# Kernel optimization log

Measured on AMD Instinct MI355X. Metric: run time of the kernel, lower is better.

## Reference

```python
import jax, jax.numpy as jnp
import numpy as np
from jax import lax

B, T, D, H = 64, 2048, 128, 256  # batch, seq_len, input_dim, hidden_dim


def setup_inputs() -> dict:
    key = jax.random.key(0)
    ks = jax.random.split(key, 21)
    s = 0.05
    p = lambda k, shape: jax.random.normal(k, shape, dtype=jnp.float32) * s
    inp = {"x": jax.random.normal(ks[0], (B, T, D), dtype=jnp.float32)}
    i = 1
    for n in ["e1", "e2", "d1", "d2"]:  # encode1, encode2, reconstruct1, reconstruct2
        inp[n + "_Wih"] = p(ks[i], (4 * H, D)); i += 1
        inp[n + "_Whh"] = p(ks[i], (4 * H, H)); i += 1
        inp[n + "_bih"] = p(ks[i], (4 * H,)); i += 1
        inp[n + "_bhh"] = p(ks[i], (4 * H,)); i += 1
    inp["l1_W"] = p(ks[17], (D, H)); inp["l1_b"] = p(ks[18], (D,))
    inp["l2_W"] = p(ks[19], (D, H)); inp["l2_b"] = p(ks[20], (D,))
    return inp


def _lstm_cell(h, c, xt, Wih, Whh, bih, bhh):
    # PyTorch gate order: i, f, g, o
    g = xt @ Wih.T + h @ Whh.T + bih + bhh  # [B, 4H]
    i, f, gg, o = jnp.split(g, 4, axis=-1)
    c = jax.nn.sigmoid(f) * c + jax.nn.sigmoid(i) * jnp.tanh(gg)
    h = jax.nn.sigmoid(o) * jnp.tanh(c)
    return h, c


def _encode(x, h0, c0, Wih, Whh, bih, bhh):
    # x: [B, T, D] batch_first -> scan over time
    def step(carry, xt):
        h, c = carry
        h, c = _lstm_cell(h, c, xt, Wih, Whh, bih, bhh)
        return (h, c), None
    (h, c), _ = lax.scan(step, (h0, c0), jnp.swapaxes(x, 0, 1))
    return h, c


def _decode(n, h, c, Wih, Whh, bih, bhh, Wl, bl):
    # first output is linear(hidden) before any cell step (matches original decode)
    inp0 = h @ Wl.T + bl  # [B, D]
    def step(carry, _):
        h, c, inp = carry
        h, c = _lstm_cell(h, c, inp, Wih, Whh, bih, bhh)
        inp = h @ Wl.T + bl
        return (h, c, inp), inp
    _, outs = lax.scan(step, (h, c, inp0), None, length=n - 1)  # [n-1, B, D]
    out = jnp.concatenate([inp0[None], outs], axis=0)  # [n, B, D]
    return jnp.swapaxes(out, 0, 1)  # [B, n, D]


def reference(x,
              e1_Wih, e1_Whh, e1_bih, e1_bhh,
              e2_Wih, e2_Whh, e2_bih, e2_bhh,
              d1_Wih, d1_Whh, d1_bih, d1_bhh,
              d2_Wih, d2_Whh, d2_bih, d2_bhh,
              l1_W, l1_b, l2_W, l2_b):
    Bc, Tc = x.shape[0], x.shape[1]
    T1 = Tc // 2
    h0 = jnp.zeros((Bc, H), dtype=x.dtype)
    c0 = jnp.zeros((Bc, H), dtype=x.dtype)
    x1 = x[:, :T1][:, ::-1]  # first half, time-reversed
    x2 = x[:, T1:]
    h1, c1 = _encode(x1, h0, c0, e1_Wih, e1_Whh, e1_bih, e1_bhh)
    h2, c2 = _encode(x2, h1, c1, e2_Wih, e2_Whh, e2_bih, e2_bhh)
    out1 = _decode(T1, h1, c1, d1_Wih, d1_Whh, d1_bih, d1_bhh, l1_W, l1_b)
    out2 = _decode(Tc - T1, h2, c2, d2_Wih, d2_Whh, d2_bih, d2_bhh, l2_W, l2_b)[:, ::-1]
    return jnp.concatenate([out1, out2], axis=1)  # [B, T, D]
```

## Files before the change

### kernel.cpp

```cpp
#include <hip/hip_runtime.h>
#include <stdint.h>

#define Bv 64
#define Tv 2048
#define T1v 1024
#define Dv 128
#define Hv 256

typedef _Float16 h2_t __attribute__((ext_vector_type(2)));

__device__ inline float d2(uint32_t hp, uint32_t wp, float acc) {
#if __has_builtin(__builtin_amdgcn_fdot2)
  return __builtin_amdgcn_fdot2(__builtin_bit_cast(h2_t, hp),
                                __builtin_bit_cast(h2_t, wp), acc, false);
#else
  float out;
  asm("v_dot2_f32_f16 %0, %1, %2, %3" : "=v"(out) : "v"(hp), "v"(wp), "v"(acc));
  return out;
#endif
}

__device__ inline uint16_t f2h(float x) {
  _Float16 h = (_Float16)x;
  return __builtin_bit_cast(uint16_t, h);
}
__device__ inline float h2f(uint16_t u) {
  return (float)__builtin_bit_cast(_Float16, u);
}
__device__ inline uint32_t packpair(float a, float b) {
  return (uint32_t)f2h(a) | ((uint32_t)f2h(b) << 16);
}


__global__ void k_pack_x(const float* __restrict__ x, uint32_t* __restrict__ xpk) {
  int idx = blockIdx.x * 256 + threadIdx.x;
  const float2* x2 = (const float2*)x;
  float2 v = x2[idx];
  xpk[idx] = packpair(v.x, v.y);
}

__global__ void k_pack_w(const float* __restrict__ src, uint32_t* __restrict__ wAll,
                         uint32_t* __restrict__ wLg, uint32_t* __restrict__ wStr) {
  int idx = blockIdx.x * 256 + threadIdx.x;
  int row = idx >> 7, k2 = idx & 127;
  uint32_t pr = packpair(src[row * 256 + 2 * k2], src[row * 256 + 2 * k2 + 1]);
  wAll[k2 * 1024 + row] = pr;
  if (k2 >= 96) {
    int g = (k2 - 96) >> 2, q = (k2 - 96) & 3;
    wLg[(g * 1024 + row) * 4 + q] = pr;
  }
  if (k2 >= 48 && k2 < 96) wStr[row * 48 + (k2 - 48)] = pr;
}

__global__ void k_pack_wih(const float* __restrict__ Wih, uint32_t* __restrict__ wihp) {
  int idx = blockIdx.x * 256 + threadIdx.x;
  int row = idx >> 6, k2 = idx & 63;
  wihp[row * 64 + k2] = packpair(Wih[row * 128 + 2 * k2], Wih[row * 128 + 2 * k2 + 1]);
}

__global__ void k_bias2(const float* __restrict__ bih, const float* __restrict__ bhh,
                        float* __restrict__ bias) {
  int i = blockIdx.x * 256 + threadIdx.x;
  if (i < 1024) bias[i] = bih[i] + bhh[i];
}

__global__ void k_dec_combine(const float* __restrict__ Whh, const float* __restrict__ Wih,
                              const float* __restrict__ bih, const float* __restrict__ bhh,
                              const float* __restrict__ lW, const float* __restrict__ lb,
                              float* __restrict__ wd, float* __restrict__ bias) {
  int j = blockIdx.x;
  int k = threadIdx.x;
  __shared__ float wr[128];
  if (k < 128) wr[k] = Wih[j * 128 + k];
  __syncthreads();
  float acc = Whh[j * 256 + k];
  for (int d = 0; d < 128; ++d) acc += wr[d] * lW[d * 256 + k];
  wd[j * 256 + k] = acc;
  if (k == 0) {
    float s = bih[j] + bhh[j];
    for (int d = 0; d < 128; ++d) s += wr[d] * lb[d];
    bias[j] = s;
  }
}

__global__ void k_pack_wl(const float* __restrict__ lW, uint32_t* __restrict__ wlp) {
  int idx = blockIdx.x * 256 + threadIdx.x;
  int d = idx >> 7, k2 = idx & 127;
  wlp[d * 128 + k2] = packpair(lW[d * 256 + 2 * k2], lW[d * 256 + 2 * k2 + 1]);
}

__global__ __launch_bounds__(256) void k_xp_gemm(const uint32_t* __restrict__ xpk,
                                                 const uint32_t* __restrict__ wihp,
                                                 uint16_t* __restrict__ xp, int xt0, int xdt) {
  const int b = blockIdx.z;
  const int s0 = blockIdx.y * 32;
  const int r = blockIdx.x * 256 + threadIdx.x;
  uint32_t wreg[64];
#pragma unroll
  for (int k = 0; k < 64; ++k) wreg[k] = wihp[r * 64 + k];
  for (int sl = 0; sl < 32; ++sl) {
    const int s = s0 + sl;
    const int t = xt0 + s * xdt;
    const uint32_t* __restrict__ xrow = xpk + ((size_t)b * Tv + t) * 64;
    float a0 = 0.f, a1 = 0.f;
#pragma unroll
    for (int k = 0; k < 64; k += 2) {
      a0 = d2(xrow[k], wreg[k], a0);
      a1 = d2(xrow[k + 1], wreg[k + 1], a1);
    }
    xp[((size_t)b * T1v + s) * 1024 + r] = f2h(a0 + a1);
  }
}


struct ChainCfg {
  const uint32_t* wAll;
  const uint4* wLg;
  const uint32_t* wStr;
  const uint32_t* wih;
  const uint32_t* xpk;
  const uint16_t* xps;
  const float* bias;
  const float* h0;
  const float* c0;
  float* hN;
  float* cN;
  uint16_t* hist;
  int xt0, xdt;
};

template <int NRESP, bool WIH>
__global__ void __launch_bounds__(512)
__attribute__((amdgpu_waves_per_eu(2, 2)))
k_rnn5(ChainCfg cA, ChainCfg cB, int nA) {
  __shared__ __align__(16) uint4 wlds4[8 * 1024];
  __shared__ float gsm[1024];
  __shared__ __align__(16) uint16_t h16[256];
  __shared__ __align__(16) uint32_t xsh[64];

  const bool isA = (int)blockIdx.x < nA;
  const ChainCfg cfg = isA ? cA : cB;
  const int b = isA ? (int)blockIdx.x : ((int)blockIdx.x - nA);
  const int tid = threadIdx.x;
  const int r0 = tid, r1 = tid + 512;

#pragma unroll
  for (int i = 0; i < 16; ++i) wlds4[i * 512 + tid] = cfg.wLg[i * 512 + tid];

  uint16_t* histp = cfg.hist ? cfg.hist + (size_t)b * 1024 * 256 : nullptr;

  float creg = 0.f;
  if (tid < 256) {
    float h0v = cfg.h0 ? cfg.h0[b * 256 + tid] : 0.f;
    creg = cfg.c0 ? cfg.c0[b * 256 + tid] : 0.f;
    uint16_t hu = f2h(h0v);
    h16[tid] = hu;
    if (histp) histp[tid] = hu;
  }

  uint32_t w0[NRESP], w1[NRESP];
#pragma unroll
  for (int k = 0; k < NRESP; ++k) w0[k] = cfg.wAll[k * 1024 + r0];
#pragma unroll
  for (int k = 0; k < NRESP; ++k) w1[k] = cfg.wAll[k * 1024 + r1];
  const float bias0 = cfg.bias[r0];
  const float bias1 = cfg.bias[r1];

  constexpr int NS4 = (96 - NRESP) / 4;
  const uint4* ws0 = (const uint4*)(cfg.wStr + (size_t)r0 * 48 + (NRESP - 48));
  const uint4* ws1 = (const uint4*)(cfg.wStr + (size_t)r1 * 48 + (NRESP - 48));
  const uint4* wi0 = cfg.wih ? (const uint4*)(cfg.wih + (size_t)r0 * 64) : nullptr;
  const uint4* wi1 = cfg.wih ? (const uint4*)(cfg.wih + (size_t)r1 * 64) : nullptr;
  const bool hasx = cfg.xps != nullptr;

  __syncthreads();

  for (int s = 0; s < 1024; ++s) {
    float xa0 = 0.f, xa1 = 0.f;
    if (hasx) {
      size_t xb = ((size_t)b * 1024 + s) * 1024;
      xa0 = h2f(cfg.xps[xb + r0]);
      xa1 = h2f(cfg.xps[xb + r1]);
    }
    if constexpr (WIH) {
      if (cfg.wih) {
        if (tid < 64) {
          const int t = cfg.xt0 + s * cfg.xdt;
          xsh[tid] = cfg.xpk[((size_t)b * Tv + t) * 64 + tid];
        }
        __syncthreads();
      }
    }

    const uint4* H4 = (const uint4*)h16;
    float a00 = bias0, a01 = 0.f, a10 = bias1, a11 = 0.f;

#pragma unroll
    for (int c4 = 0; c4 < NRESP / 4; ++c4) {
      const uint4 hv = H4[c4];
      a00 = d2(hv.x, w0[4 * c4 + 0], a00);
      a01 = d2(hv.y, w0[4 * c4 + 1], a01);
      a10 = d2(hv.x, w1[4 * c4 + 0], a10);
      a11 = d2(hv.y, w1[4 * c4 + 1], a11);
      a00 = d2(hv.z, w0[4 * c4 + 2], a00);
      a01 = d2(hv.w, w0[4 * c4 + 3], a01);
      a10 = d2(hv.z, w1[4 * c4 + 2], a10);
      a11 = d2(hv.w, w1[4 * c4 + 3], a11);
    }
    if constexpr (NS4 > 0) {
#pragma unroll
      for (int u = 0; u < NS4; ++u) {
        const uint4 hv = H4[NRESP / 4 + u];
        const uint4 wv0 = ws0[u];
        const uint4 wv1 = ws1[u];
        a00 = d2(hv.x, wv0.x, a00);
        a01 = d2(hv.y, wv0.y, a01);
        a10 = d2(hv.x, wv1.x, a10);
        a11 = d2(hv.y, wv1.y, a11);
        a00 = d2(hv.z, wv0.z, a00);
        a01 = d2(hv.w, wv0.w, a01);
        a10 = d2(hv.z, wv1.z, a10);
        a11 = d2(hv.w, wv1.w, a11);
      }
    }
#pragma unroll
    for (int g = 0; g < 8; ++g) {
      const uint4 hv = H4[24 + g];
      const uint4 wv0 = wlds4[g * 1024 + r0];
      const uint4 wv1 = wlds4[g * 1024 + r1];
      a00 = d2(hv.x, wv0.x, a00);
      a01 = d2(hv.y, wv0.y, a01);
      a10 = d2(hv.x, wv1.x, a10);
      a11 = d2(hv.y, wv1.y, a11);
      a00 = d2(hv.z, wv0.z, a00);
      a01 = d2(hv.w, wv0.w, a01);
      a10 = d2(hv.z, wv1.z, a10);
      a11 = d2(hv.w, wv1.w, a11);
    }
    if constexpr (WIH) {
      if (cfg.wih) {
        const uint4* XS4 = (const uint4*)xsh;
#pragma unroll
        for (int u = 0; u < 16; ++u) {
          const uint4 xv = XS4[u];
          const uint4 wv0 = wi0[u];
          const uint4 wv1 = wi1[u];
          a00 = d2(xv.x, wv0.x, a00);
          a01 = d2(xv.y, wv0.y, a01);
          a10 = d2(xv.x, wv1.x, a10);
          a11 = d2(xv.y, wv1.y, a11);
          a00 = d2(xv.z, wv0.z, a00);
          a01 = d2(xv.w, wv0.w, a01);
          a10 = d2(xv.z, wv1.z, a10);
          a11 = d2(xv.w, wv1.w, a11);
        }
      }
    }

    gsm[r0] = a00 + a01 + xa0;
    gsm[r1] = a10 + a11 + xa1;
    __syncthreads();

    if (tid < 256) {
      const float gi = gsm[tid];
      const float gf = gsm[tid + 256];
      const float gg = gsm[tid + 512];
      const float go = gsm[tid + 768];
      const float si = 1.f / (1.f + __expf(-gi));
      const float sf = 1.f / (1.f + __expf(-gf));
      const float so = 1.f / (1.f + __expf(-go));
      const float tg = 2.f / (1.f + __expf(-2.f * gg)) - 1.f;
      const float cn = sf * creg + si * tg;
      const float tc = 2.f / (1.f + __expf(-2.f * cn)) - 1.f;
      creg = cn;
      const uint16_t hu = f2h(so * tc);
      h16[tid] = hu;
      if (histp && s < 1023) histp[(size_t)(s + 1) * 256 + tid] = hu;
    }
    __syncthreads();
  }

  if (cfg.hN && tid < 256) {
    cfg.hN[b * 256 + tid] = h2f(h16[tid]);
    cfg.cN[b * 256 + tid] = creg;
  }
}

template <bool WIH>
__global__ void __launch_bounds__(1024) k_rnnD(ChainCfg cA, ChainCfg cB, int nA) {
  __shared__ __align__(16) uint4 wlds4[8 * 1024];
  __shared__ float gsm[1024];
  __shared__ __align__(16) uint16_t h16[256];
  __shared__ __align__(16) uint32_t xsh[64];

  const bool isA = (int)blockIdx.x < nA;
  const ChainCfg cfg = isA ? cA : cB;
  const int b = isA ? (int)blockIdx.x : ((int)blockIdx.x - nA);
  const int tid = threadIdx.x;
  const int r0 = tid;

#pragma unroll
  for (int i = 0; i < 8; ++i) wlds4[i * 1024 + tid] = cfg.wLg[i * 1024 + tid];

  uint16_t* histp = cfg.hist ? cfg.hist + (size_t)b * 1024 * 256 : nullptr;

  float creg = 0.f;
  if (tid < 256) {
    float h0v = cfg.h0 ? cfg.h0[b * 256 + tid] : 0.f;
    creg = cfg.c0 ? cfg.c0[b * 256 + tid] : 0.f;
    uint16_t hu = f2h(h0v);
    h16[tid] = hu;
    if (histp) histp[tid] = hu;
  }

  uint32_t w0[48];
#pragma unroll
  for (int k = 0; k < 48; ++k) w0[k] = cfg.wAll[k * 1024 + r0];
  const float bias0 = cfg.bias[r0];
  const uint4* ws0 = (const uint4*)(cfg.wStr + (size_t)r0 * 48);
  const uint4* wi0 = cfg.wih ? (const uint4*)(cfg.wih + (size_t)r0 * 64) : nullptr;
  const bool hasx = cfg.xps != nullptr;

  __syncthreads();

  for (int s = 0; s < 1024; ++s) {
    float xa0 = 0.f;
    if (hasx) xa0 = h2f(cfg.xps[((size_t)b * 1024 + s) * 1024 + r0]);
    if constexpr (WIH) {
      if (cfg.wih) {
        if (tid < 64) {
          const int t = cfg.xt0 + s * cfg.xdt;
          xsh[tid] = cfg.xpk[((size_t)b * Tv + t) * 64 + tid];
        }
        __syncthreads();
      }
    }

    const uint4* H4 = (const uint4*)h16;
    float a00 = bias0, a01 = 0.f;
#pragma unroll
    for (int c4 = 0; c4 < 12; ++c4) {
      const uint4 hv = H4[c4];
      a00 = d2(hv.x, w0[4 * c4 + 0], a00);
      a01 = d2(hv.y, w0[4 * c4 + 1], a01);
      a00 = d2(hv.z, w0[4 * c4 + 2], a00);
      a01 = d2(hv.w, w0[4 * c4 + 3], a01);
    }
#pragma unroll 4
    for (int u = 0; u < 12; ++u) {
      const uint4 hv = H4[12 + u];
      const uint4 wv = ws0[u];
      a00 = d2(hv.x, wv.x, a00);
      a01 = d2(hv.y, wv.y, a01);
      a00 = d2(hv.z, wv.z, a00);
      a01 = d2(hv.w, wv.w, a01);
    }
#pragma unroll
    for (int g = 0; g < 8; ++g) {
      const uint4 hv = H4[24 + g];
      const uint4 wv = wlds4[g * 1024 + r0];
      a00 = d2(hv.x, wv.x, a00);
      a01 = d2(hv.y, wv.y, a01);
      a00 = d2(hv.z, wv.z, a00);
      a01 = d2(hv.w, wv.w, a01);
    }
    if constexpr (WIH) {
      if (cfg.wih) {
        const uint4* XS4 = (const uint4*)xsh;
#pragma unroll 4
        for (int u = 0; u < 16; ++u) {
          const uint4 xv = XS4[u];
          const uint4 wv = wi0[u];
          a00 = d2(xv.x, wv.x, a00);
          a01 = d2(xv.y, wv.y, a01);
          a00 = d2(xv.z, wv.z, a00);
          a01 = d2(xv.w, wv.w, a01);
        }
      }
    }

    gsm[r0] = a00 + a01 + xa0;
    __syncthreads();

    if (tid < 256) {
      const float gi = gsm[tid];
      const float gf = gsm[tid + 256];
      const float gg = gsm[tid + 512];
      const float go = gsm[tid + 768];
      const float si = 1.f / (1.f + __expf(-gi));
      const float sf = 1.f / (1.f + __expf(-gf));
      const float so = 1.f / (1.f + __expf(-go));
      const float tg = 2.f / (1.f + __expf(-2.f * gg)) - 1.f;
      const float cn = sf * creg + si * tg;
      const float tc = 2.f / (1.f + __expf(-2.f * cn)) - 1.f;
      creg = cn;
      const uint16_t hu = f2h(so * tc);
      h16[tid] = hu;
      if (histp && s < 1023) histp[(size_t)(s + 1) * 256 + tid] = hu;
    }
    __syncthreads();
  }

  if (cfg.hN && tid < 256) {
    cfg.hN[b * 256 + tid] = h2f(h16[tid]);
    cfg.cN[b * 256 + tid] = creg;
  }
}

__global__ __launch_bounds__(256) void k_out(const uint16_t* __restrict__ hist,
                                             const uint32_t* __restrict__ wlp,
                                             const float* __restrict__ lb,
                                             float* __restrict__ out, int outbase, int tsign) {
  const int b = blockIdx.y;
  const int t0 = blockIdx.x * 64;
  __shared__ __align__(16) uint32_t hq[64 * 128];
  const uint32_t* hsrc = (const uint32_t*)hist;
  for (int i = threadIdx.x; i < 64 * 128; i += 256) {
    hq[i] = hsrc[((size_t)b * 1024 + t0) * 128 + i];
  }
  __syncthreads();
  const int d = threadIdx.x & 127;
  const int th = threadIdx.x >> 7;
  float acc[32];
#pragma unroll
  for (int it = 0; it < 32; ++it) acc[it] = lb[d];
  const uint4* W4 = (const uint4*)(wlp + (size_t)d * 128);
  const uint4* HQ4 = (const uint4*)hq;
  for (int k2c = 0; k2c < 32; ++k2c) {
    const uint4 wv = W4[k2c];
#pragma unroll
    for (int it = 0; it < 32; ++it) {
      const int tl = th * 32 + it;
      const uint4 hv = HQ4[tl * 32 + k2c];
      acc[it] = d2(hv.x, wv.x, acc[it]);
      acc[it] = d2(hv.y, wv.y, acc[it]);
      acc[it] = d2(hv.z, wv.z, acc[it]);
      acc[it] = d2(hv.w, wv.w, acc[it]);
    }
  }
#pragma unroll
  for (int it = 0; it < 32; ++it) {
    const int tl = th * 32 + it;
    const int t = t0 + tl;
    const int tout = outbase + tsign * t;
    out[((size_t)b * Tv + tout) * Dv + d] = acc[it];
  }
}


extern "C" void kernel_launch(void* const* d_in, const int* in_sizes, int n_in,
                              void* d_out, int out_size, void* d_ws, size_t ws_size,
                              hipStream_t stream) {
  const float* x = (const float*)d_in[0];
  const float* e1_Wih = (const float*)d_in[1];
  const float* e1_Whh = (const float*)d_in[2];
  const float* e1_bih = (const float*)d_in[3];
  const float* e1_bhh = (const float*)d_in[4];
  const float* e2_Wih = (const float*)d_in[5];
  const float* e2_Whh = (const float*)d_in[6];
  const float* e2_bih = (const float*)d_in[7];
  const float* e2_bhh = (const float*)d_in[8];
  const float* d1_Wih = (const float*)d_in[9];
  const float* d1_Whh = (const float*)d_in[10];
  const float* d1_bih = (const float*)d_in[11];
  const float* d1_bhh = (const float*)d_in[12];
  const float* d2_Wih = (const float*)d_in[13];
  const float* d2_Whh = (const float*)d_in[14];
  const float* d2_bih = (const float*)d_in[15];
  const float* d2_bhh = (const float*)d_in[16];
  const float* l1_W = (const float*)d_in[17];
  const float* l1_b = (const float*)d_in[18];
  const float* l2_W = (const float*)d_in[19];
  const float* l2_b = (const float*)d_in[20];

  uint8_t* wsb = (uint8_t*)d_ws;
  size_t off = 0;
  auto take = [&](size_t n) -> void* {
    void* pp = wsb + off;
    off += (n + 255) & ~(size_t)255;
    return pp;
  };
  uint32_t* xpk = (uint32_t*)take((size_t)Bv * Tv * 64 * 4);
  uint16_t* hist1 = (uint16_t*)take((size_t)Bv * T1v * Hv * 2);
  uint16_t* hist2 = (uint16_t*)take((size_t)Bv * T1v * Hv * 2);
  struct WSet { uint32_t *wAll, *wLg, *wStr, *wih; float* bias; };
  auto take_wset = [&](bool with_ih) -> WSet {
    WSet w;
    w.wAll = (uint32_t*)take(128 * 1024 * 4);
    w.wLg = (uint32_t*)take(8 * 1024 * 16);
    w.wStr = (uint32_t*)take(1024 * 48 * 4);
    w.wih = with_ih ? (uint32_t*)take(1024 * 64 * 4) : nullptr;
    w.bias = (float*)take(1024 * 4);
    return w;
  };
  WSet we1 = take_wset(true);
  WSet we2 = take_wset(true);
  WSet wd1 = take_wset(false);
  WSet wd2 = take_wset(false);
  float* wd32 = (float*)take(1024 * 256 * 4);
  uint32_t* wl1p = (uint32_t*)take(128 * 128 * 4);
  uint32_t* wl2p = (uint32_t*)take(128 * 128 * 4);
  float* h1 = (float*)take(64 * 256 * 4);
  float* c1 = (float*)take(64 * 256 * 4);
  float* h2 = (float*)take(64 * 256 * 4);
  float* c2 = (float*)take(64 * 256 * 4);
  uint16_t* xp = (uint16_t*)take((size_t)Bv * T1v * 1024 * 2);
  const bool use_xp = ws_size >= off;

  int variant = 2;
  {
    hipFuncAttributes fa;
    auto ok = [&](const void* f) {
      return hipFuncGetAttributes(&fa, f) == hipSuccess && fa.localSizeBytes == 0;
    };
    if (use_xp) {
      if (ok(reinterpret_cast<const void*>(&k_rnn5<96, false>))) variant = 0;
      else if (ok(reinterpret_cast<const void*>(&k_rnn5<80, false>))) variant = 1;
    } else {
      if (ok(reinterpret_cast<const void*>(&k_rnn5<96, true>))) variant = 0;
      else if (ok(reinterpret_cast<const void*>(&k_rnn5<80, true>))) variant = 1;
    }
  }
  auto launch_rnn = [&](int grid, ChainCfg a, ChainCfg b2, int nA) {
    if (use_xp) {
      if (variant == 0)      k_rnn5<96, false><<<grid, 512, 0, stream>>>(a, b2, nA);
      else if (variant == 1) k_rnn5<80, false><<<grid, 512, 0, stream>>>(a, b2, nA);
      else                   k_rnnD<false><<<grid, 1024, 0, stream>>>(a, b2, nA);
    } else {
      if (variant == 0)      k_rnn5<96, true><<<grid, 512, 0, stream>>>(a, b2, nA);
      else if (variant == 1) k_rnn5<80, true><<<grid, 512, 0, stream>>>(a, b2, nA);
      else                   k_rnnD<true><<<grid, 1024, 0, stream>>>(a, b2, nA);
    }
  };

  k_pack_x<<<(Bv * Tv * 64) / 256, 256, 0, stream>>>(x, xpk);
  k_pack_w<<<512, 256, 0, stream>>>(e1_Whh, we1.wAll, we1.wLg, we1.wStr);
  k_pack_wih<<<256, 256, 0, stream>>>(e1_Wih, we1.wih);
  k_bias2<<<4, 256, 0, stream>>>(e1_bih, e1_bhh, we1.bias);
  k_pack_w<<<512, 256, 0, stream>>>(e2_Whh, we2.wAll, we2.wLg, we2.wStr);
  k_pack_wih<<<256, 256, 0, stream>>>(e2_Wih, we2.wih);
  k_bias2<<<4, 256, 0, stream>>>(e2_bih, e2_bhh, we2.bias);
  k_dec_combine<<<1024, 256, 0, stream>>>(d1_Whh, d1_Wih, d1_bih, d1_bhh, l1_W, l1_b, wd32, wd1.bias);
  k_pack_w<<<512, 256, 0, stream>>>(wd32, wd1.wAll, wd1.wLg, wd1.wStr);
  k_dec_combine<<<1024, 256, 0, stream>>>(d2_Whh, d2_Wih, d2_bih, d2_bhh, l2_W, l2_b, wd32, wd2.bias);
  k_pack_w<<<512, 256, 0, stream>>>(wd32, wd2.wAll, wd2.wLg, wd2.wStr);
  k_pack_wl<<<64, 256, 0, stream>>>(l1_W, wl1p);
  k_pack_wl<<<64, 256, 0, stream>>>(l2_W, wl2p);

  if (use_xp) k_xp_gemm<<<dim3(4, 32, 64), 256, 0, stream>>>(xpk, we1.wih, xp, 1023, -1);
  ChainCfg e1c{we1.wAll, (const uint4*)we1.wLg, we1.wStr, use_xp ? nullptr : we1.wih,
               use_xp ? nullptr : xpk, use_xp ? xp : nullptr, we1.bias,
               nullptr, nullptr, h1, c1, nullptr, 1023, -1};
  launch_rnn(64, e1c, e1c, 64);

  if (use_xp) k_xp_gemm<<<dim3(4, 32, 64), 256, 0, stream>>>(xpk, we2.wih, xp, 1024, 1);
  ChainCfg e2c{we2.wAll, (const uint4*)we2.wLg, we2.wStr, use_xp ? nullptr : we2.wih,
               use_xp ? nullptr : xpk, use_xp ? xp : nullptr, we2.bias,
               h1, c1, h2, c2, nullptr, 1024, 1};
  ChainCfg d1c{wd1.wAll, (const uint4*)wd1.wLg, wd1.wStr, nullptr, nullptr, nullptr,
               wd1.bias, h1, c1, nullptr, nullptr, hist1, 0, 0};
  launch_rnn(128, e2c, d1c, 64);

  ChainCfg d2c{wd2.wAll, (const uint4*)wd2.wLg, wd2.wStr, nullptr, nullptr, nullptr,
               wd2.bias, h2, c2, nullptr, nullptr, hist2, 0, 0};
  launch_rnn(64, d2c, d2c, 64);

  k_out<<<dim3(16, 64), 256, 0, stream>>>(hist1, wl1p, l1_b, (float*)d_out, 0, 1);
  k_out<<<dim3(16, 64), 256, 0, stream>>>(hist2, wl2p, l2_b, (float*)d_out, 2047, -1);
}
```

Baseline: 7.015 ms.

## Add 512-thread LSTM recurrence kernel with per-unit gate ownership and DPP reductions

Adds a new recurrent kernel in which each group of four threads owns two hidden units across all four gates. The K dimension is split four ways and reduced with DPP cross-lane adds, so the gate activations run in registers without a shared-memory gate buffer. The h vector is double-buffered, leaving one barrier per step instead of two. Weights are repacked so 192 words per thread live in VGPRs and the rest in LDS, and the input projection is stored in a matching interleaved layout. This risks heavy register pressure, which is why it sits behind a spill check with fallback to the old kernel, and it removes the 1024-thread fallback path.

```diff
diff --git a/kernel.cpp b/kernel.cpp
--- a/kernel.cpp
+++ b/kernel.cpp
@@ -30,6 +30,18 @@
 __device__ inline uint32_t packpair(float a, float b) {
   return (uint32_t)f2h(a) | ((uint32_t)f2h(b) << 16);
 }
+__device__ inline float unpk(uint32_t u, int hi) {
+  return h2f((uint16_t)(hi ? (u >> 16) : (u & 0xffff)));
+}
+__device__ inline float sigm(float x) { return 1.f / (1.f + __expf(-x)); }
+__device__ inline float tanh_(float x) { return 2.f / (1.f + __expf(-2.f * x)) - 1.f; }
+
+__device__ inline float qsum4(float v) {
+  int t = __builtin_amdgcn_update_dpp(0, __float_as_int(v), 0xB1, 0xF, 0xF, true);
+  v += __int_as_float(t);
+  t = __builtin_amdgcn_update_dpp(0, __float_as_int(v), 0x4E, 0xF, 0xF, true);
+  return v + __int_as_float(t);
+}
 
 
 __global__ void k_pack_x(const float* __restrict__ x, uint32_t* __restrict__ xpk) {
@@ -46,10 +58,42 @@
   uint32_t pr = packpair(src[row * 256 + 2 * k2], src[row * 256 + 2 * k2 + 1]);
   wAll[k2 * 1024 + row] = pr;
   if (k2 >= 96) {
-    int g = (k2 - 96) >> 2, q = (k2 - 96) & 3;
-    wLg[(g * 1024 + row) * 4 + q] = pr;
+    int g = (k2 - 96) >> 2, qq = (k2 - 96) & 3;
+    wLg[(g * 1024 + row) * 4 + qq] = pr;
   }
   if (k2 >= 48 && k2 < 96) wStr[row * 48 + (k2 - 48)] = pr;
+}
+
+__global__ void k_pack_w2(const float* __restrict__ src, uint32_t* __restrict__ wOn,
+                          uint32_t* __restrict__ wLds) {
+  int idx = blockIdx.x * 256 + threadIdx.x;
+  int r = idx >> 7, k2 = idx & 127;
+  uint32_t pr = packpair(src[r * 256 + 2 * k2], src[r * 256 + 2 * k2 + 1]);
+  int gate = r >> 8, u = r & 255;
+  int u_hi = u >> 7, jb = u & 127;
+  int q = k2 >> 5, kk = k2 & 31;
+  int tid = jb * 4 + q;
+  int ri = u_hi * 4 + gate;
+  if (kk < 24) {
+    wOn[(ri * 24 + kk) * 512 + tid] = pr;
+  } else {
+    int p = ri * 2 + ((kk - 24) >> 2);
+    int c = (kk - 24) & 3;
+    wLds[((size_t)p * 512 + tid) * 4 + c] = pr;
+  }
+}
+
+__global__ void k_bias_pack(const float* __restrict__ b32, uint32_t* __restrict__ bpk) {
+  int jb = threadIdx.x;
+  uint32_t w[4];
+#pragma unroll
+  for (int wi = 0; wi < 4; ++wi) {
+    int ri0 = 2 * wi, ri1 = 2 * wi + 1;
+    int row0 = (ri0 & 3) * 256 + jb + 128 * (ri0 >> 2);
+    int row1 = (ri1 & 3) * 256 + jb + 128 * (ri1 >> 2);
+    w[wi] = packpair(b32[row0], b32[row1]);
+  }
+  ((uint4*)bpk)[jb] = make_uint4(w[0], w[1], w[2], w[3]);
 }
 
 __global__ void k_pack_wih(const float* __restrict__ Wih, uint32_t* __restrict__ wihp) {
@@ -89,6 +133,7 @@
   wlp[d * 128 + k2] = packpair(lW[d * 256 + 2 * k2], lW[d * 256 + 2 * k2 + 1]);
 }
 
+template <int LAY>
 __global__ __launch_bounds__(256) void k_xp_gemm(const uint32_t* __restrict__ xpk,
                                                  const uint32_t* __restrict__ wihp,
                                                  uint16_t* __restrict__ xp, int xt0, int xdt) {
@@ -98,6 +143,9 @@
   uint32_t wreg[64];
 #pragma unroll
   for (int k = 0; k < 64; ++k) wreg[k] = wihp[r * 64 + k];
+  const int gate = r >> 8, u = r & 255;
+  const int u_hi = u >> 7, jb = u & 127;
+  const int ri = u_hi * 4 + gate;
   for (int sl = 0; sl < 32; ++sl) {
     const int s = s0 + sl;
     const int t = xt0 + s * xdt;
@@ -108,7 +156,136 @@
       a0 = d2(xrow[k], wreg[k], a0);
       a1 = d2(xrow[k + 1], wreg[k + 1], a1);
     }
-    xp[((size_t)b * T1v + s) * 1024 + r] = f2h(a0 + a1);
+    uint16_t v = f2h(a0 + a1);
+    if (LAY == 0)
+      xp[(((size_t)b * T1v + s) * 128 + jb) * 8 + ri] = v;
+    else
+      xp[((size_t)b * T1v + s) * 1024 + r] = v;
+  }
+}
+
+
+struct CfgU {
+  const uint32_t* wOn;
+  const uint4* wLds;
+  const uint4* bpk;
+  const uint4* xps;
+  const float* h0;
+  const float* c0;
+  float* hN;
+  float* cN;
+  uint16_t* hist;
+};
+
+__global__ void __launch_bounds__(512)
+__attribute__((amdgpu_waves_per_eu(2, 2)))
+k_rnnU(CfgU cA, CfgU cB, int nA) {
+  __shared__ __align__(16) uint4 wldsM[16 * 512];
+  __shared__ __align__(16) uint16_t hb[2][256];
+
+  const bool isA = (int)blockIdx.x < nA;
+  const CfgU cfg = isA ? cA : cB;
+  const int b = isA ? (int)blockIdx.x : ((int)blockIdx.x - nA);
+  const int tid = threadIdx.x;
+  const int q = tid & 3, jb = tid >> 2;
+  const float qz = (q == 0) ? 1.f : 0.f;
+
+#pragma unroll
+  for (int i = 0; i < 16; ++i) wldsM[i * 512 + tid] = cfg.wLds[i * 512 + tid];
+
+  uint32_t wreg[192];
+#pragma unroll
+  for (int k = 0; k < 192; ++k) wreg[k] = cfg.wOn[k * 512 + tid];
+
+  const uint4 bp = cfg.bpk[jb];
+  float c0r = cfg.c0 ? cfg.c0[b * 256 + jb] : 0.f;
+  float c1r = cfg.c0 ? cfg.c0[b * 256 + jb + 128] : 0.f;
+
+  uint16_t* histp = cfg.hist ? cfg.hist + (size_t)b * 1024 * 256 : nullptr;
+  if (q == 0) {
+    float h00 = cfg.h0 ? cfg.h0[b * 256 + jb] : 0.f;
+    float h01 = cfg.h0 ? cfg.h0[b * 256 + jb + 128] : 0.f;
+    uint16_t u0 = f2h(h00), u1 = f2h(h01);
+    hb[0][jb] = u0;
+    hb[0][jb + 128] = u1;
+    if (histp) {
+      histp[jb] = u0;
+      histp[jb + 128] = u1;
+    }
+  }
+  const uint4* xps4 = cfg.xps ? cfg.xps + (size_t)b * 1024 * 128 + jb : nullptr;
+
+  __syncthreads();
+
+  int cur = 0;
+  for (int s = 0; s < 1024; ++s) {
+    uint4 xq = make_uint4(0, 0, 0, 0);
+    if (xps4) xq = xps4[(size_t)s * 128];
+
+    float acc[8];
+    acc[0] = qz * (unpk(bp.x, 0) + unpk(xq.x, 0));
+    acc[1] = qz * (unpk(bp.x, 1) + unpk(xq.x, 1));
+    acc[2] = qz * (unpk(bp.y, 0) + unpk(xq.y, 0));
+    acc[3] = qz * (unpk(bp.y, 1) + unpk(xq.y, 1));
+    acc[4] = qz * (unpk(bp.z, 0) + unpk(xq.z, 0));
+    acc[5] = qz * (unpk(bp.z, 1) + unpk(xq.z, 1));
+    acc[6] = qz * (unpk(bp.w, 0) + unpk(xq.w, 0));
+    acc[7] = qz * (unpk(bp.w, 1) + unpk(xq.w, 1));
+
+    const uint4* H4 = (const uint4*)hb[cur];
+#pragma unroll
+    for (int c = 0; c < 6; ++c) {
+      const uint4 hv = H4[q * 8 + c];
+#pragma unroll
+      for (int ri = 0; ri < 8; ++ri) {
+        const int base = ri * 24 + c * 4;
+        acc[ri] = d2(hv.x, wreg[base + 0], acc[ri]);
+        acc[ri] = d2(hv.y, wreg[base + 1], acc[ri]);
+        acc[ri] = d2(hv.z, wreg[base + 2], acc[ri]);
+        acc[ri] = d2(hv.w, wreg[base + 3], acc[ri]);
+      }
+    }
+#pragma unroll
+    for (int p = 0; p < 2; ++p) {
+      const uint4 hv = H4[q * 8 + 6 + p];
+#pragma unroll
+      for (int ri = 0; ri < 8; ++ri) {
+        const uint4 wv = wldsM[(ri * 2 + p) * 512 + tid];
+        acc[ri] = d2(hv.x, wv.x, acc[ri]);
+        acc[ri] = d2(hv.y, wv.y, acc[ri]);
+        acc[ri] = d2(hv.z, wv.z, acc[ri]);
+        acc[ri] = d2(hv.w, wv.w, acc[ri]);
+      }
+    }
+
+#pragma unroll
+    for (int ri = 0; ri < 8; ++ri) acc[ri] = qsum4(acc[ri]);
+
+    const float cn0 = sigm(acc[1]) * c0r + sigm(acc[0]) * tanh_(acc[2]);
+    const float h0v = sigm(acc[3]) * tanh_(cn0);
+    c0r = cn0;
+    const float cn1 = sigm(acc[5]) * c1r + sigm(acc[4]) * tanh_(acc[6]);
+    const float h1v = sigm(acc[7]) * tanh_(cn1);
+    c1r = cn1;
+
+    const uint16_t hu0 = f2h(h0v), hu1 = f2h(h1v);
+    if (q == 0) {
+      hb[cur ^ 1][jb] = hu0;
+      hb[cur ^ 1][jb + 128] = hu1;
+      if (histp && s < 1023) {
+        histp[(size_t)(s + 1) * 256 + jb] = hu0;
+        histp[(size_t)(s + 1) * 256 + jb + 128] = hu1;
+      }
+    }
+    __syncthreads();
+    cur ^= 1;
+  }
+
+  if (cfg.hN && q == 0) {
+    cfg.hN[b * 256 + jb] = h2f(hb[cur][jb]);
+    cfg.hN[b * 256 + jb + 128] = h2f(hb[cur][jb + 128]);
+    cfg.cN[b * 256 + jb] = c0r;
+    cfg.cN[b * 256 + jb + 128] = c1r;
   }
 }
 
@@ -266,135 +443,10 @@
       const float gf = gsm[tid + 256];
       const float gg = gsm[tid + 512];
       const float go = gsm[tid + 768];
-      const float si = 1.f / (1.f + __expf(-gi));
-      const float sf = 1.f / (1.f + __expf(-gf));
-      const float so = 1.f / (1.f + __expf(-go));
-      const float tg = 2.f / (1.f + __expf(-2.f * gg)) - 1.f;
-      const float cn = sf * creg + si * tg;
-      const float tc = 2.f / (1.f + __expf(-2.f * cn)) - 1.f;
+      const float cn = sigm(gf) * creg + sigm(gi) * tanh_(gg);
+      const float hv = sigm(go) * tanh_(cn);
       creg = cn;
-      const uint16_t hu = f2h(so * tc);
-      h16[tid] = hu;
-      if (histp && s < 1023) histp[(size_t)(s + 1) * 256 + tid] = hu;
-    }
-    __syncthreads();
-  }
-
-  if (cfg.hN && tid < 256) {
-    cfg.hN[b * 256 + tid] = h2f(h16[tid]);
-    cfg.cN[b * 256 + tid] = creg;
-  }
-}
-
-template <bool WIH>
-__global__ void __launch_bounds__(1024) k_rnnD(ChainCfg cA, ChainCfg cB, int nA) {
-  __shared__ __align__(16) uint4 wlds4[8 * 1024];
-  __shared__ float gsm[1024];
-  __shared__ __align__(16) uint16_t h16[256];
-  __shared__ __align__(16) uint32_t xsh[64];
-
-  const bool isA = (int)blockIdx.x < nA;
-  const ChainCfg cfg = isA ? cA : cB;
-  const int b = isA ? (int)blockIdx.x : ((int)blockIdx.x - nA);
-  const int tid = threadIdx.x;
-  const int r0 = tid;
-
-#pragma unroll
-  for (int i = 0; i < 8; ++i) wlds4[i * 1024 + tid] = cfg.wLg[i * 1024 + tid];
-
-  uint16_t* histp = cfg.hist ? cfg.hist + (size_t)b * 1024 * 256 : nullptr;
-
-  float creg = 0.f;
-  if (tid < 256) {
-    float h0v = cfg.h0 ? cfg.h0[b * 256 + tid] : 0.f;
-    creg = cfg.c0 ? cfg.c0[b * 256 + tid] : 0.f;
-    uint16_t hu = f2h(h0v);
-    h16[tid] = hu;
-    if (histp) histp[tid] = hu;
-  }
-
-  uint32_t w0[48];
-#pragma unroll
-  for (int k = 0; k < 48; ++k) w0[k] = cfg.wAll[k * 1024 + r0];
-  const float bias0 = cfg.bias[r0];
-  const uint4* ws0 = (const uint4*)(cfg.wStr + (size_t)r0 * 48);
-  const uint4* wi0 = cfg.wih ? (const uint4*)(cfg.wih + (size_t)r0 * 64) : nullptr;
-  const bool hasx = cfg.xps != nullptr;
-
-  __syncthreads();
-
-  for (int s = 0; s < 1024; ++s) {
-    float xa0 = 0.f;
-    if (hasx) xa0 = h2f(cfg.xps[((size_t)b * 1024 + s) * 1024 + r0]);
-    if constexpr (WIH) {
-      if (cfg.wih) {
-        if (tid < 64) {
-          const int t = cfg.xt0 + s * cfg.xdt;
-          xsh[tid] = cfg.xpk[((size_t)b * Tv + t) * 64 + tid];
-        }
-        __syncthreads();
-      }
-    }
-
-    const uint4* H4 = (const uint4*)h16;
-    float a00 = bias0, a01 = 0.f;
-#pragma unroll
-    for (int c4 = 0; c4 < 12; ++c4) {
-      const uint4 hv = H4[c4];
-      a00 = d2(hv.x, w0[4 * c4 + 0], a00);
-      a01 = d2(hv.y, w0[4 * c4 + 1], a01);
-      a00 = d2(hv.z, w0[4 * c4 + 2], a00);
-      a01 = d2(hv.w, w0[4 * c4 + 3], a01);
-    }
-#pragma unroll 4
-    for (int u = 0; u < 12; ++u) {
-      const uint4 hv = H4[12 + u];
-      const uint4 wv = ws0[u];
-      a00 = d2(hv.x, wv.x, a00);
-      a01 = d2(hv.y, wv.y, a01);
-      a00 = d2(hv.z, wv.z, a00);
-      a01 = d2(hv.w, wv.w, a01);
-    }
-#pragma unroll
-    for (int g = 0; g < 8; ++g) {
-      const uint4 hv = H4[24 + g];
-      const uint4 wv = wlds4[g * 1024 + r0];
-      a00 = d2(hv.x, wv.x, a00);
-      a01 = d2(hv.y, wv.y, a01);
-      a00 = d2(hv.z, wv.z, a00);
-      a01 = d2(hv.w, wv.w, a01);
-    }
-    if constexpr (WIH) {
-      if (cfg.wih) {
-        const uint4* XS4 = (const uint4*)xsh;
-#pragma unroll 4
-        for (int u = 0; u < 16; ++u) {
-          const uint4 xv = XS4[u];
-          const uint4 wv = wi0[u];
-          a00 = d2(xv.x, wv.x, a00);
-          a01 = d2(xv.y, wv.y, a01);
-          a00 = d2(xv.z, wv.z, a00);
-          a01 = d2(xv.w, wv.w, a01);
-        }
-      }
-    }
-
-    gsm[r0] = a00 + a01 + xa0;
-    __syncthreads();
-
-    if (tid < 256) {
-      const float gi = gsm[tid];
-      const float gf = gsm[tid + 256];
-      const float gg = gsm[tid + 512];
-      const float go = gsm[tid + 768];
-      const float si = 1.f / (1.f + __expf(-gi));
-      const float sf = 1.f / (1.f + __expf(-gf));
-      const float so = 1.f / (1.f + __expf(-go));
-      const float tg = 2.f / (1.f + __expf(-2.f * gg)) - 1.f;
-      const float cn = sf * creg + si * tg;
-      const float tc = 2.f / (1.f + __expf(-2.f * cn)) - 1.f;
-      creg = cn;
-      const uint16_t hu = f2h(so * tc);
+      const uint16_t hu = f2h(hv);
       h16[tid] = hu;
       if (histp && s < 1023) histp[(size_t)(s + 1) * 256 + tid] = hu;
     }
@@ -483,7 +535,11 @@
   uint32_t* xpk = (uint32_t*)take((size_t)Bv * Tv * 64 * 4);
   uint16_t* hist1 = (uint16_t*)take((size_t)Bv * T1v * Hv * 2);
   uint16_t* hist2 = (uint16_t*)take((size_t)Bv * T1v * Hv * 2);
-  struct WSet { uint32_t *wAll, *wLg, *wStr, *wih; float* bias; };
+  struct WSet {
+    uint32_t *wAll, *wLg, *wStr, *wih;
+    float* bias;
+    uint32_t *wOn, *wLds, *bpk;
+  };
   auto take_wset = [&](bool with_ih) -> WSet {
     WSet w;
     w.wAll = (uint32_t*)take(128 * 1024 * 4);
@@ -491,6 +547,9 @@
     w.wStr = (uint32_t*)take(1024 * 48 * 4);
     w.wih = with_ih ? (uint32_t*)take(1024 * 64 * 4) : nullptr;
     w.bias = (float*)take(1024 * 4);
+    w.wOn = (uint32_t*)take(192 * 512 * 4);
+    w.wLds = (uint32_t*)take(16 * 512 * 16);
+    w.bpk = (uint32_t*)take(128 * 16);
     return w;
   };
   WSet we1 = take_wset(true);
@@ -510,60 +569,85 @@
   int variant = 2;
   {
     hipFuncAttributes fa;
-    auto ok = [&](const void* f) {
+    auto spillfree = [&](const void* f) {
       return hipFuncGetAttributes(&fa, f) == hipSuccess && fa.localSizeBytes == 0;
     };
-    if (use_xp) {
-      if (ok(reinterpret_cast<const void*>(&k_rnn5<96, false>))) variant = 0;
-      else if (ok(reinterpret_cast<const void*>(&k_rnn5<80, false>))) variant = 1;
+    if (use_xp && spillfree(reinterpret_cast<const void*>(&k_rnnU))) {
+      variant = 0;
+    } else if (use_xp) {
+      if (spillfree(reinterpret_cast<const void*>(&k_rnn5<96, false>))) variant = 1;
     } else {
-      if (ok(reinterpret_cast<const void*>(&k_rnn5<96, true>))) variant = 0;
-      else if (ok(reinterpret_cast<const void*>(&k_rnn5<80, true>))) variant = 1;
-    }
-  }
-  auto launch_rnn = [&](int grid, ChainCfg a, ChainCfg b2, int nA) {
-    if (use_xp) {
-      if (variant == 0)      k_rnn5<96, false><<<grid, 512, 0, stream>>>(a, b2, nA);
-      else if (variant == 1) k_rnn5<80, false><<<grid, 512, 0, stream>>>(a, b2, nA);
-      else                   k_rnnD<false><<<grid, 1024, 0, stream>>>(a, b2, nA);
-    } else {
-      if (variant == 0)      k_rnn5<96, true><<<grid, 512, 0, stream>>>(a, b2, nA);
-      else if (variant == 1) k_rnn5<80, true><<<grid, 512, 0, stream>>>(a, b2, nA);
-      else                   k_rnnD<true><<<grid, 1024, 0, stream>>>(a, b2, nA);
-    }
-  };
+      if (spillfree(reinterpret_cast<const void*>(&k_rnn5<96, true>))) variant = 1;
+    }
+  }
 
   k_pack_x<<<(Bv * Tv * 64) / 256, 256, 0, stream>>>(x, xpk);
   k_pack_w<<<512, 256, 0, stream>>>(e1_Whh, we1.wAll, we1.wLg, we1.wStr);
+  k_pack_w2<<<512, 256, 0, stream>>>(e1_Whh, we1.wOn, we1.wLds);
   k_pack_wih<<<256, 256, 0, stream>>>(e1_Wih, we1.wih);
   k_bias2<<<4, 256, 0, stream>>>(e1_bih, e1_bhh, we1.bias);
+  k_bias_pack<<<1, 128, 0, stream>>>(we1.bias, we1.bpk);
   k_pack_w<<<512, 256, 0, stream>>>(e2_Whh, we2.wAll, we2.wLg, we2.wStr);
+  k_pack_w2<<<512, 256, 0, stream>>>(e2_Whh, we2.wOn, we2.wLds);
   k_pack_wih<<<256, 256, 0, stream>>>(e2_Wih, we2.wih);
   k_bias2<<<4, 256, 0, stream>>>(e2_bih, e2_bhh, we2.bias);
+  k_bias_pack<<<1, 128, 0, stream>>>(we2.bias, we2.bpk);
   k_dec_combine<<<1024, 256, 0, stream>>>(d1_Whh, d1_Wih, d1_bih, d1_bhh, l1_W, l1_b, wd32, wd1.bias);
   k_pack_w<<<512, 256, 0, stream>>>(wd32, wd1.wAll, wd1.wLg, wd1.wStr);
+  k_pack_w2<<<512, 256, 0, stream>>>(wd32, wd1.wOn, wd1.wLds);
+  k_bias_pack<<<1, 128, 0, stream>>>(wd1.bias, wd1.bpk);
   k_dec_combine<<<1024, 256, 0, stream>>>(d2_Whh, d2_Wih, d2_bih, d2_bhh, l2_W, l2_b, wd32, wd2.bias);
   k_pack_w<<<512, 256, 0, stream>>>(wd32, wd2.wAll, wd2.wLg, wd2.wStr);
+  k_pack_w2<<<512, 256, 0, stream>>>(wd32, wd2.wOn, wd2.wLds);
+  k_bias_pack<<<1, 128, 0, stream>>>(wd2.bias, wd2.bpk);
   k_pack_wl<<<64, 256, 0, stream>>>(l1_W, wl1p);
   k_pack_wl<<<64, 256, 0, stream>>>(l2_W, wl2p);
 
-  if (use_xp) k_xp_gemm<<<dim3(4, 32, 64), 256, 0, stream>>>(xpk, we1.wih, xp, 1023, -1);
-  ChainCfg e1c{we1.wAll, (const uint4*)we1.wLg, we1.wStr, use_xp ? nullptr : we1.wih,
-               use_xp ? nullptr : xpk, use_xp ? xp : nullptr, we1.bias,
-               nullptr, nullptr, h1, c1, nullptr, 1023, -1};
-  launch_rnn(64, e1c, e1c, 64);
-
-  if (use_xp) k_xp_gemm<<<dim3(4, 32, 64), 256, 0, stream>>>(xpk, we2.wih, xp, 1024, 1);
-  ChainCfg e2c{we2.wAll, (const uint4*)we2.wLg, we2.wStr, use_xp ? nullptr : we2.wih,
-               use_xp ? nullptr : xpk, use_xp ? xp : nullptr, we2.bias,
-               h1, c1, h2, c2, nullptr, 1024, 1};
-  ChainCfg d1c{wd1.wAll, (const uint4*)wd1.wLg, wd1.wStr, nullptr, nullptr, nullptr,
-               wd1.bias, h1, c1, nullptr, nullptr, hist1, 0, 0};
-  launch_rnn(128, e2c, d1c, 64);
-
-  ChainCfg d2c{wd2.wAll, (const uint4*)wd2.wLg, wd2.wStr, nullptr, nullptr, nullptr,
-               wd2.bias, h2, c2, nullptr, nullptr, hist2, 0, 0};
-  launch_rnn(64, d2c, d2c, 64);
+  auto launch_old = [&](int grid, ChainCfg a, ChainCfg b2, int nA) {
+    if (use_xp) {
+      if (variant == 1) k_rnn5<96, false><<<grid, 512, 0, stream>>>(a, b2, nA);
+      else              k_rnn5<80, false><<<grid, 512, 0, stream>>>(a, b2, nA);
+    } else {
+      if (variant == 1) k_rnn5<96, true><<<grid, 512, 0, stream>>>(a, b2, nA);
+      else              k_rnn5<80, true><<<grid, 512, 0, stream>>>(a, b2, nA);
+    }
+  };
+
+  if (variant == 0) {
+    k_xp_gemm<0><<<dim3(4, 32, 64), 256, 0, stream>>>(xpk, we1.wih, xp, 1023, -1);
+    CfgU e1c{we1.wOn, (const uint4*)we1.wLds, (const uint4*)we1.bpk, (const uint4*)xp,
+             nullptr, nullptr, h1, c1, nullptr};
+    k_rnnU<<<64, 512, 0, stream>>>(e1c, e1c, 64);
+
+    k_xp_gemm<0><<<dim3(4, 32, 64), 256, 0, stream>>>(xpk, we2.wih, xp, 1024, 1);
+    CfgU e2c{we2.wOn, (const uint4*)we2.wLds, (const uint4*)we2.bpk, (const uint4*)xp,
+             h1, c1, h2, c2, nullptr};
+    CfgU d1c{wd1.wOn, (const uint4*)wd1.wLds, (const uint4*)wd1.bpk, nullptr,
+             h1, c1, nullptr, nullptr, hist1};
+    k_rnnU<<<128, 512, 0, stream>>>(e2c, d1c, 64);
+
+    CfgU d2c{wd2.wOn, (const uint4*)wd2.wLds, (const uint4*)wd2.bpk, nullptr,
+             h2, c2, nullptr, nullptr, hist2};
+    k_rnnU<<<64, 512, 0, stream>>>(d2c, d2c, 64);
+  } else {
+    if (use_xp) k_xp_gemm<1><<<dim3(4, 32, 64), 256, 0, stream>>>(xpk, we1.wih, xp, 1023, -1);
+    ChainCfg e1c{we1.wAll, (const uint4*)we1.wLg, we1.wStr, use_xp ? nullptr : we1.wih,
+                 use_xp ? nullptr : xpk, use_xp ? xp : nullptr, we1.bias,
+                 nullptr, nullptr, h1, c1, nullptr, 1023, -1};
+    launch_old(64, e1c, e1c, 64);
+
+    if (use_xp) k_xp_gemm<1><<<dim3(4, 32, 64), 256, 0, stream>>>(xpk, we2.wih, xp, 1024, 1);
+    ChainCfg e2c{we2.wAll, (const uint4*)we2.wLg, we2.wStr, use_xp ? nullptr : we2.wih,
+                 use_xp ? nullptr : xpk, use_xp ? xp : nullptr, we2.bias,
+                 h1, c1, h2, c2, nullptr, 1024, 1};
+    ChainCfg d1c{wd1.wAll, (const uint4*)wd1.wLg, wd1.wStr, nullptr, nullptr, nullptr,
+                 wd1.bias, h1, c1, nullptr, nullptr, hist1, 0, 0};
+    launch_old(128, e2c, d1c, 64);
+
+    ChainCfg d2c{wd2.wAll, (const uint4*)wd2.wLg, wd2.wStr, nullptr, nullptr, nullptr,
+                 wd2.bias, h2, c2, nullptr, nullptr, hist2, 0, 0};
+    launch_old(64, d2c, d2c, 64);
+  }
 
   k_out<<<dim3(16, 64), 256, 0, stream>>>(hist1, wl1p, l1_b, (float*)d_out, 0, 1);
   k_out<<<dim3(16, 64), 256, 0, stream>>>(hist2, wl2p, l2_b, (float*)d_out, 2047, -1);
```

Measured after the change: 7.022 ms. Within noise of the previous version (+0.1%).
